# Kernel optimization log

Measured on AMD Instinct MI355X. Metric: run time of the kernel, lower is better.

## Reference

```python
import jax, jax.numpy as jnp
import numpy as np

B, T, RES, C = 4, 8, 32, 128
TSP, SPLIT = 4, 4
NH_BRANCH = 4  # num_heads // 2 per branch
HID = 4 * C


def layer_norm(x, w, b, eps=1e-5):
    mu = x.mean(-1, keepdims=True)
    var = ((x - mu) ** 2).mean(-1, keepdims=True)
    return (x - mu) * jax.lax.rsqrt(var + eps) * w + b


def dwconv3d(x, w, b):
    # x: (Bw, C, Tsp, Hsp, Wsp); w: (C, 1, 3, 3, 3) depthwise
    y = jax.lax.conv_general_dilated(
        x, w, (1, 1, 1), 'SAME',
        dimension_numbers=('NCDHW', 'OIDHW', 'NCDHW'),
        feature_group_count=x.shape[1])
    return y + b[None, :, None, None, None]


def lepe_attention(q, k, v, conv_w, conv_b, Tsp, Hsp, Wsp, nh, Tt, H, W):
    Bq, L, Cc = q.shape
    hd = Cc // nh
    win = Tsp * Hsp * Wsp
    scale = float(hd) ** -0.5

    def to_win(z):
        z = z.reshape(Bq, Tt // Tsp, Tsp, H // Hsp, Hsp, W // Wsp, Wsp, Cc)
        z = z.transpose(0, 1, 3, 5, 2, 4, 6, 7).reshape(-1, win, nh, hd)
        return z.transpose(0, 2, 1, 3)

    qw = to_win(q) * scale
    kw = to_win(k)
    # v windows as (Bw, C, Tsp, Hsp, Wsp) for the depthwise-conv LePE
    vw5 = v.reshape(Bq, Tt // Tsp, Tsp, H // Hsp, Hsp, W // Wsp, Wsp, Cc)
    vw5 = vw5.transpose(0, 1, 3, 5, 7, 2, 4, 6).reshape(-1, Cc, Tsp, Hsp, Wsp)
    lepe = dwconv3d(vw5, conv_w, conv_b)

    def heads(z5):
        return z5.reshape(-1, nh, hd, win).transpose(0, 1, 3, 2)

    vh, lepeh = heads(vw5), heads(lepe)
    attn = jax.nn.softmax(jnp.einsum('bnqd,bnkd->bnqk', qw, kw), axis=-1)
    out = jnp.einsum('bnqk,bnkd->bnqd', attn, vh) + lepeh
    # windows -> video token order (T, H, W)
    out = out.transpose(0, 2, 1, 3).reshape(
        Bq, Tt // Tsp, H // Hsp, W // Wsp, Tsp, Hsp, Wsp, Cc)
    out = out.transpose(0, 1, 4, 2, 5, 3, 6, 7).reshape(Bq, L, Cc)
    return out


def setup_inputs() -> dict:
    key = jax.random.key(0)
    ks = jax.random.split(key, 16)
    L = T * RES * RES
    h = C // 2
    p = lambda k, s: jax.random.normal(k, s, dtype=jnp.float32) * 0.02
    return {
        'x': jax.random.normal(ks[0], (B, L, C), dtype=jnp.float32),
        'norm1_w': jnp.ones((C,), jnp.float32),
        'norm1_b': jnp.zeros((C,), jnp.float32),
        'qkv_w': p(ks[1], (3 * C, C)),
        'conv_w0': p(ks[2], (h, 1, 3, 3, 3)),
        'conv_b0': jnp.zeros((h,), jnp.float32),
        'conv_w1': p(ks[3], (h, 1, 3, 3, 3)),
        'conv_b1': jnp.zeros((h,), jnp.float32),
        'proj_w': p(ks[4], (C, C)),
        'proj_b': jnp.zeros((C,), jnp.float32),
        'norm2_w': jnp.ones((C,), jnp.float32),
        'norm2_b': jnp.zeros((C,), jnp.float32),
        'fc1_w': p(ks[5], (HID, C)),
        'fc1_b': jnp.zeros((HID,), jnp.float32),
        'fc2_w': p(ks[6], (C, HID)),
        'fc2_b': jnp.zeros((C,), jnp.float32),
    }


def reference(x, norm1_w, norm1_b, qkv_w, conv_w0, conv_b0, conv_w1, conv_b1,
              proj_w, proj_b, norm2_w, norm2_b, fc1_w, fc1_b, fc2_w, fc2_b):
    img = layer_norm(x, norm1_w, norm1_b)
    qkv = img @ qkv_w.T  # (B, L, 3C), split order q, k, v
    q, k, v = jnp.split(qkv, 3, axis=-1)
    h = C // 2
    # branch 0 (idx=0): H_sp = reso, W_sp = split_size
    x1 = lepe_attention(q[..., :h], k[..., :h], v[..., :h], conv_w0, conv_b0,
                        TSP, RES, SPLIT, NH_BRANCH, T, RES, RES)
    # branch 1 (idx=1): H_sp = split_size, W_sp = reso
    x2 = lepe_attention(q[..., h:], k[..., h:], v[..., h:], conv_w1, conv_b1,
                        TSP, SPLIT, RES, NH_BRANCH, T, RES, RES)
    att = jnp.concatenate([x1, x2], axis=2) @ proj_w.T + proj_b
    x = x + att
    y = layer_norm(x, norm2_w, norm2_b)
    y = jax.nn.gelu(y @ fc1_w.T + fc1_b, approximate=False) @ fc2_w.T + fc2_b
    return x + y
```

## Files before the change

kernel.cpp:

```cpp
#include <hip/hip_runtime.h>
#include <math.h>

namespace {
constexpr int C_ = 128;
constexpr int BL = 32768;
constexpr int LS = 140;

typedef __attribute__((ext_vector_type(4))) float f32x4;
typedef __attribute__((ext_vector_type(4))) _Float16 f16x4;
typedef __attribute__((ext_vector_type(8))) _Float16 f16x8;
typedef __attribute__((ext_vector_type(2))) __fp16 hf2;

#if __has_builtin(__builtin_amdgcn_exp2f)
#define EXP2F(x) __builtin_amdgcn_exp2f(x)
#else
#define EXP2F(x) exp2f(x)
#endif
}

__global__ __launch_bounds__(256) void k_cvt(
    const float* __restrict__ qkvw, const float* __restrict__ pw,
    const float* __restrict__ f1w,  const float* __restrict__ f2w,
    const float* __restrict__ cw0,  const float* __restrict__ cw1,
    _Float16* __restrict__ wqh, _Float16* __restrict__ pwh,
    _Float16* __restrict__ w1h, _Float16* __restrict__ w2h,
    float* __restrict__ lepw)
{
  int i = blockIdx.x * 256 + threadIdx.x;
  if (i < 49152) {
    float v = qkvw[i];
    if (i < 16384) v *= 0.360673762f;
    wqh[i] = (_Float16)v;
  }
  else if (i < 65536)  pwh[i - 49152] = (_Float16)pw[i - 49152];
  else if (i < 131072) w1h[i - 65536] = (_Float16)f1w[i - 65536];
  else if (i < 196608) w2h[i - 131072] = (_Float16)f2w[i - 131072];
  else if (i < 200064) {
    int j = i - 196608;
    int br = j / 1728, r = j % 1728, widx = r >> 6, ch = r & 63;
    lepw[j] = (br ? cw1 : cw0)[ch * 27 + widx];
  }
}

__global__ __launch_bounds__(512) void k_ln_qkv(
    const float* __restrict__ x,
    const float* __restrict__ nw,
    const float* __restrict__ nb,
    const _Float16* __restrict__ wqh,
    _Float16* __restrict__ qh, _Float16* __restrict__ kh, _Float16* __restrict__ vh)
{
  __shared__ _Float16 xs[64][LS];
  __shared__ _Float16 qt[64][LS];
  __shared__ _Float16 wbuf[128][LS];
  const int tid = threadIdx.x;
  const int row0 = blockIdx.x << 6;
  const int bb = row0 >> 13, t = (row0 >> 10) & 7, h0 = (row0 >> 5) & 31;
  const int tb = t >> 2, t_in = t & 3;

  {
    const int r = tid >> 3, j = tid & 7;
    const float* xp = x + (size_t)(row0 + r) * C_ + j * 16;
    float v[16];
#pragma unroll
    for (int i = 0; i < 4; ++i) {
      float4 u = ((const float4*)xp)[i];
      v[i*4+0] = u.x; v[i*4+1] = u.y; v[i*4+2] = u.z; v[i*4+3] = u.w;
    }
    float s1 = 0.f, s2 = 0.f;
#pragma unroll
    for (int i = 0; i < 16; ++i) { s1 += v[i]; s2 += v[i] * v[i]; }
    s1 += __shfl_down(s1, 4, 8); s1 += __shfl_down(s1, 2, 8); s1 += __shfl_down(s1, 1, 8);
    s2 += __shfl_down(s2, 4, 8); s2 += __shfl_down(s2, 2, 8); s2 += __shfl_down(s2, 1, 8);
    float mu = __shfl(s1, 0, 8) * (1.f / 128.f);
    float ms = __shfl(s2, 0, 8) * (1.f / 128.f);
    float rstd = rsqrtf(ms - mu * mu + 1e-5f);
#pragma unroll
    for (int i = 0; i < 16; ++i) {
      int c = j * 16 + i;
      xs[r][c] = (_Float16)((v[i] - mu) * rstd * nw[c] + nb[c]);
    }
  }
  __syncthreads();

  const int lane = tid & 63, wave = tid >> 6;
  const int mq = wave & 3, nh = wave >> 2;
  const int m0 = mq << 4, mi = lane & 15, quad = lane >> 4;

  f16x8 afr[4];
#pragma unroll
  for (int kt = 0; kt < 4; ++kt)
    afr[kt] = *(const f16x8*)&xs[m0 + mi][kt * 32 + quad * 8];

  for (int g = 0; g < 3; ++g) {
#pragma unroll
    for (int it = 0; it < 4; ++it) {
      int id = it * 512 + tid;
      int r = id >> 4, c8 = id & 15;
      *(uint4*)&wbuf[r][c8 * 8] = *(const uint4*)(wqh + (size_t)(g * 128 + r) * 128 + c8 * 8);
    }
    __syncthreads();

    f32x4 acc[4];
#pragma unroll
    for (int nt = 0; nt < 4; ++nt) acc[nt] = (f32x4){0.f, 0.f, 0.f, 0.f};
#pragma unroll
    for (int nt = 0; nt < 4; ++nt) {
      int wrow = (nh * 4 + nt) * 16 + mi;
#pragma unroll
      for (int kt = 0; kt < 4; ++kt) {
        f16x8 bfr = *(const f16x8*)&wbuf[wrow][kt * 32 + quad * 8];
        acc[nt] = __builtin_amdgcn_mfma_f32_16x16x32_f16(afr[kt], bfr, acc[nt], 0, 0, 0);
      }
    }
#pragma unroll
    for (int nt = 0; nt < 4; ++nt) {
      int n = (nh * 4 + nt) * 16 + mi;
#pragma unroll
      for (int rr = 0; rr < 4; ++rr)
        qt[m0 + quad * 4 + rr][n] = (_Float16)acc[nt][rr];
    }
    __syncthreads();

    _Float16* G = (g == 0) ? qh : (g == 1) ? kh : vh;
#pragma unroll
    for (int it = 0; it < 2; ++it) {
      int u = it * 512 + tid;
      if (u < 512) {
        int half = u & 1, p = (u >> 1) & 7, head = (u >> 4) & 3, sb = u >> 6;
        int token = (p >> 2) * 32 + sb * 4 + (p & 3);
        uint4 d = *(const uint4*)&qt[token][head * 16 + half * 8];
        int win = bb * 16 + tb * 8 + sb;
        int pos = t_in * 128 + h0 * 4 + p;
        *(uint4*)(G + ((size_t)(head * 64 + win) * 512 + pos) * 16 + half * 8) = d;
      } else {
        int u2 = u - 512;
        int half = u2 & 1, pin = (u2 >> 1) & 63, head = u2 >> 7;
        uint4 d = *(const uint4*)&qt[pin][64 + head * 16 + half * 8];
        int win = bb * 16 + tb * 8 + (h0 >> 2);
        int pos = t_in * 128 + (h0 & 3) * 32 + pin;
        *(uint4*)(G + ((size_t)((4 + head) * 64 + win) * 512 + pos) * 16 + half * 8) = d;
      }
    }
    __syncthreads();
  }
}

__global__ __launch_bounds__(512) void k_attn(
    const _Float16* __restrict__ qh,
    const _Float16* __restrict__ kh,
    const _Float16* __restrict__ vh,
    const float* __restrict__ lepw,
    const float* __restrict__ cb0,
    const float* __restrict__ cb1,
    _Float16* __restrict__ attnh)
{
  __shared__ _Float16 Ks[512][20];
  __shared__ _Float16 Vs[512][20];
  __shared__ _Float16 Vt[16][520];

  const int tid = threadIdx.x;
  const int bid = blockIdx.x;
  const int br = bid >> 8, wi = (bid >> 2) & 63, head = bid & 3;
  const int b = wi >> 4, tb = (wi >> 3) & 1, sb = wi & 7;
  const int coff = br * 64 + head * 16;
  const int Hsp = br ? 4 : 32, Wsp = br ? 32 : 4;
  const float* cb = br ? cb1 : cb0;
  const size_t base = ((size_t)(br * 4 + head) * 64 + wi) * 512 * 16;

  auto token_of = [&](int p) -> int {
    int t_in = p >> 7;
    int rem = p & 127;
    int h, w;
    if (br == 0) { h = rem >> 2;            w = sb * 4 + (rem & 3); }
    else         { h = sb * 4 + (rem >> 5); w = rem & 31; }
    return ((b * 8 + tb * 4 + t_in) << 10) + (h << 5) + w;
  };

  {
    const int r = tid;
    const _Float16* kp = kh + base + r * 16;
    const _Float16* vp = vh + base + r * 16;
    f16x8 k0 = *(const f16x8*)kp;
    f16x8 k1 = *(const f16x8*)(kp + 8);
    f16x8 v0 = *(const f16x8*)vp;
    f16x8 v1 = *(const f16x8*)(vp + 8);
    *(f16x4*)&Ks[r][0]  = (f16x4){k0[0], k0[1], k0[2], k0[3]};
    *(f16x4*)&Ks[r][4]  = (f16x4){k0[4], k0[5], k0[6], k0[7]};
    *(f16x4*)&Ks[r][8]  = (f16x4){k1[0], k1[1], k1[2], k1[3]};
    *(f16x4*)&Ks[r][12] = (f16x4){k1[4], k1[5], k1[6], k1[7]};
    *(f16x4*)&Vs[r][0]  = (f16x4){v0[0], v0[1], v0[2], v0[3]};
    *(f16x4*)&Vs[r][4]  = (f16x4){v0[4], v0[5], v0[6], v0[7]};
    *(f16x4*)&Vs[r][8]  = (f16x4){v1[0], v1[1], v1[2], v1[3]};
    *(f16x4*)&Vs[r][12] = (f16x4){v1[4], v1[5], v1[6], v1[7]};
#pragma unroll
    for (int d = 0; d < 8; ++d) { Vt[d][r] = v0[d]; Vt[d + 8][r] = v1[d]; }
  }

  const int lane = tid & 63, wave = tid >> 6;
  const int mi = lane & 15, quad = lane >> 4;

  int qtok[4];
  f16x4 qfr[4];
#pragma unroll
  for (int qi = 0; qi < 4; ++qi) {
    int q = (wave * 4 + qi) * 16 + mi;
    qtok[qi] = token_of(q);
    qfr[qi] = *(const f16x4*)(qh + base + q * 16 + quad * 4);
  }
  __syncthreads();

  f32x4 acc[4];
  float l[4];
#pragma unroll
  for (int qi = 0; qi < 4; ++qi) { acc[qi] = (f32x4){0.f,0.f,0.f,0.f}; l[qi] = 0.f; }

  const hf2 one2 = {(__fp16)1.f, (__fp16)1.f};

  for (int kt = 0; kt < 32; ++kt) {
    const int kb = kt << 4;
    f16x4 kfr = *(const f16x4*)&Ks[kb + mi][quad * 4];
    f16x4 vfr = *(const f16x4*)&Vt[mi][kb + quad * 4];
#pragma unroll
    for (int qi = 0; qi < 4; ++qi) {
      f32x4 s = __builtin_amdgcn_mfma_f32_16x16x16f16(kfr, qfr[qi], (f32x4){0.f,0.f,0.f,0.f}, 0, 0, 0);
      float p0 = EXP2F(s[0]);
      float p1 = EXP2F(s[1]);
      float p2 = EXP2F(s[2]);
      float p3 = EXP2F(s[3]);
      hf2 plo = __builtin_amdgcn_cvt_pkrtz(p0, p1);
      hf2 phi = __builtin_amdgcn_cvt_pkrtz(p2, p3);
#if __has_builtin(__builtin_amdgcn_fdot2)
      l[qi] = __builtin_amdgcn_fdot2(plo, one2, l[qi], false);
      l[qi] = __builtin_amdgcn_fdot2(phi, one2, l[qi], false);
#else
      l[qi] += (p0 + p1) + (p2 + p3);
#endif
      union { struct { hf2 lo, hi; } h; f16x4 v; } u;
      u.h.lo = plo; u.h.hi = phi;
      acc[qi] = __builtin_amdgcn_mfma_f32_16x16x16f16(vfr, u.v, acc[qi], 0, 0, 0);
    }
  }

#pragma unroll
  for (int qi = 0; qi < 4; ++qi) {
    float lq = l[qi];
    lq += __shfl_xor(lq, 16, 64);
    lq += __shfl_xor(lq, 32, 64);
    float inv = 1.f / lq;

    const int q = (wave * 4 + qi) * 16 + mi;
    int t_in = q >> 7, rem = q & 127;
    int h_in, w_in;
    if (br == 0) { h_in = rem >> 2; w_in = rem & 3; }
    else         { h_in = rem >> 5; w_in = rem & 31; }
    float4 lep = *(const float4*)(cb + head * 16 + quad * 4);
    for (int dz = 0; dz < 3; ++dz) {
      int tz = t_in + dz - 1; if ((unsigned)tz >= 4u) continue;
      for (int dy = 0; dy < 3; ++dy) {
        int ty = h_in + dy - 1; if ((unsigned)ty >= (unsigned)Hsp) continue;
        for (int dx = 0; dx < 3; ++dx) {
          int tx = w_in + dx - 1; if ((unsigned)tx >= (unsigned)Wsp) continue;
          int np = (tz * Hsp + ty) * Wsp + tx;
          int widx = (dz * 3 + dy) * 3 + dx;
          float4 w4 = *(const float4*)(lepw + ((br * 27 + widx) << 6) + head * 16 + quad * 4);
          f16x4 vv = *(const f16x4*)&Vs[np][quad * 4];
          lep.x += w4.x * (float)vv[0];
          lep.y += w4.y * (float)vv[1];
          lep.z += w4.z * (float)vv[2];
          lep.w += w4.w * (float)vv[3];
        }
      }
    }
    f16x4 ov;
    ov[0] = (_Float16)(acc[qi][0] * inv + lep.x);
    ov[1] = (_Float16)(acc[qi][1] * inv + lep.y);
    ov[2] = (_Float16)(acc[qi][2] * inv + lep.z);
    ov[3] = (_Float16)(acc[qi][3] * inv + lep.w);
    *(f16x4*)(attnh + (size_t)qtok[qi] * 128 + coff + quad * 4) = ov;
  }
}

__global__ __launch_bounds__(512) void k_proj(
    const _Float16* __restrict__ attnh,
    const _Float16* __restrict__ pwh,
    const float* __restrict__ pb,
    const float* __restrict__ x,
    _Float16* __restrict__ xrh)
{
  __shared__ _Float16 as_[64][LS];
  __shared__ _Float16 wbuf[128][LS];
  const int tid = threadIdx.x;
  const int row0 = blockIdx.x << 6;

#pragma unroll
  for (int it = 0; it < 2; ++it) {
    int id = it * 512 + tid;
    int r = id >> 4, c8 = id & 15;
    *(uint4*)&as_[r][c8 * 8] = *(const uint4*)(attnh + (size_t)(row0 + r) * 128 + c8 * 8);
  }
#pragma unroll
  for (int it = 0; it < 4; ++it) {
    int id = it * 512 + tid;
    int r = id >> 4, c8 = id & 15;
    *(uint4*)&wbuf[r][c8 * 8] = *(const uint4*)(pwh + (size_t)r * 128 + c8 * 8);
  }
  __syncthreads();

  const int lane = tid & 63, wave = tid >> 6;
  const int mq = wave & 3, nh = wave >> 2;
  const int m0 = mq << 4, mi = lane & 15, quad = lane >> 4;

  f16x8 afr[4];
#pragma unroll
  for (int kt = 0; kt < 4; ++kt)
    afr[kt] = *(const f16x8*)&as_[m0 + mi][kt * 32 + quad * 8];

  f32x4 acc[4];
#pragma unroll
  for (int nt = 0; nt < 4; ++nt) acc[nt] = (f32x4){0.f, 0.f, 0.f, 0.f};
#pragma unroll
  for (int nt = 0; nt < 4; ++nt) {
    int wrow = (nh * 4 + nt) * 16 + mi;
#pragma unroll
    for (int kt = 0; kt < 4; ++kt) {
      f16x8 bfr = *(const f16x8*)&wbuf[wrow][kt * 32 + quad * 8];
      acc[nt] = __builtin_amdgcn_mfma_f32_16x16x32_f16(afr[kt], bfr, acc[nt], 0, 0, 0);
    }
  }
  __syncthreads();
#pragma unroll
  for (int nt = 0; nt < 4; ++nt) {
    int n = (nh * 4 + nt) * 16 + mi;
    float bb = pb[n];
#pragma unroll
    for (int rr = 0; rr < 4; ++rr)
      as_[m0 + quad * 4 + rr][n] = (_Float16)(acc[nt][rr] + bb);
  }
  __syncthreads();

#pragma unroll
  for (int it = 0; it < 2; ++it) {
    int id = it * 512 + tid;
    int r = id >> 4, c8 = id & 15;
    f16x8 v = *(const f16x8*)&as_[r][c8 * 8];
    const float* xp = x + (size_t)(row0 + r) * 128 + c8 * 8;
    float4 xa = *(const float4*)xp;
    float4 xb = *(const float4*)(xp + 4);
    f16x8 o;
    o[0] = (_Float16)((float)v[0] + xa.x); o[1] = (_Float16)((float)v[1] + xa.y);
    o[2] = (_Float16)((float)v[2] + xa.z); o[3] = (_Float16)((float)v[3] + xa.w);
    o[4] = (_Float16)((float)v[4] + xb.x); o[5] = (_Float16)((float)v[5] + xb.y);
    o[6] = (_Float16)((float)v[6] + xb.z); o[7] = (_Float16)((float)v[7] + xb.w);
    *(f16x8*)(xrh + (size_t)(row0 + r) * 128 + c8 * 8) = o;
  }
}

__global__ __launch_bounds__(512) void k_mlp(
    const _Float16* __restrict__ xrh,
    const float* __restrict__ nw,
    const float* __restrict__ nb,
    const _Float16* __restrict__ w1h,
    const float* __restrict__ f1b,
    const _Float16* __restrict__ w2h,
    const float* __restrict__ f2b,
    float* __restrict__ out)
{
  __shared__ _Float16 xs[64][LS];
  __shared__ _Float16 wbuf[128][LS];
  const int tid = threadIdx.x;
  const int row0 = blockIdx.x << 6;

  {
    const int r = tid >> 3, j = tid & 7;
    const _Float16* xp = xrh + (size_t)(row0 + r) * C_ + j * 16;
    float v[16];
#pragma unroll
    for (int i = 0; i < 2; ++i) {
      f16x8 u = ((const f16x8*)xp)[i];
#pragma unroll
      for (int k = 0; k < 8; ++k) v[i * 8 + k] = (float)u[k];
    }
    float s1 = 0.f, s2 = 0.f;
#pragma unroll
    for (int i = 0; i < 16; ++i) { s1 += v[i]; s2 += v[i] * v[i]; }
    s1 += __shfl_down(s1, 4, 8); s1 += __shfl_down(s1, 2, 8); s1 += __shfl_down(s1, 1, 8);
    s2 += __shfl_down(s2, 4, 8); s2 += __shfl_down(s2, 2, 8); s2 += __shfl_down(s2, 1, 8);
    float mu = __shfl(s1, 0, 8) * (1.f / 128.f);
    float ms = __shfl(s2, 0, 8) * (1.f / 128.f);
    float rstd = rsqrtf(ms - mu * mu + 1e-5f);
#pragma unroll
    for (int i = 0; i < 16; ++i) {
      int c = j * 16 + i;
      xs[r][c] = (_Float16)((v[i] - mu) * rstd * nw[c] + nb[c]);
    }
  }
  __syncthreads();

  const int lane = tid & 63, wave = tid >> 6;
  const int mt = wave & 3, hh = wave >> 2;
  const int tok0 = mt << 4, mi = lane & 15, quad = lane >> 4;

  f16x8 bx[4];
#pragma unroll
  for (int kt = 0; kt < 4; ++kt)
    bx[kt] = *(const f16x8*)&xs[tok0 + mi][kt * 32 + quad * 8];

  f32x4 oacc[8];
#pragma unroll
  for (int o = 0; o < 8; ++o) oacc[o] = (f32x4){0.f, 0.f, 0.f, 0.f};

  auto gelu = [](float h) -> float {
    return h * __frcp_rn(1.f + EXP2F(-2.4554774f * h));
  };

  for (int ng = 0; ng < 4; ++ng) {
#pragma unroll
    for (int it = 0; it < 4; ++it) {
      int id = it * 512 + tid;
      int r = id >> 4, c8 = id & 15;
      *(uint4*)&wbuf[r][c8 * 8] = *(const uint4*)(w1h + (size_t)(ng * 128 + r) * 128 + c8 * 8);
    }
    __syncthreads();

    f32x4 hacc[4];
#pragma unroll
    for (int t = 0; t < 4; ++t) hacc[t] = (f32x4){0.f, 0.f, 0.f, 0.f};
#pragma unroll
    for (int t = 0; t < 4; ++t) {
      int hrow = hh * 64 + t * 16 + mi;
#pragma unroll
      for (int kt = 0; kt < 4; ++kt) {
        f16x8 wfr = *(const f16x8*)&wbuf[hrow][kt * 32 + quad * 8];
        hacc[t] = __builtin_amdgcn_mfma_f32_16x16x32_f16(wfr, bx[kt], hacc[t], 0, 0, 0);
      }
    }
    f16x4 ph[4];
#pragma unroll
    for (int t = 0; t < 4; ++t) {
      float4 bj = *(const float4*)(f1b + ng * 128 + hh * 64 + t * 16 + quad * 4);
      ph[t][0] = (_Float16)gelu(hacc[t][0] + bj.x);
      ph[t][1] = (_Float16)gelu(hacc[t][1] + bj.y);
      ph[t][2] = (_Float16)gelu(hacc[t][2] + bj.z);
      ph[t][3] = (_Float16)gelu(hacc[t][3] + bj.w);
    }
    __syncthreads();

#pragma unroll
    for (int it = 0; it < 4; ++it) {
      int id = it * 512 + tid;
      int r = id >> 4, c8 = id & 15;
      *(uint4*)&wbuf[r][c8 * 8] = *(const uint4*)(w2h + (size_t)r * 512 + ng * 128 + c8 * 8);
    }
    __syncthreads();

#pragma unroll
    for (int o = 0; o < 8; ++o) {
#pragma unroll
      for (int t = 0; t < 4; ++t) {
        f16x4 wfr = *(const f16x4*)&wbuf[o * 16 + mi][(hh * 4 + t) * 16 + quad * 4];
        oacc[o] = __builtin_amdgcn_mfma_f32_16x16x16f16(wfr, ph[t], oacc[o], 0, 0, 0);
      }
    }
    __syncthreads();
  }

  float* rbuf = (float*)wbuf;
  if (hh == 1) {
#pragma unroll
    for (int o = 0; o < 8; ++o)
#pragma unroll
      for (int k = 0; k < 4; ++k)
        rbuf[(o * 4 + k) * 256 + mt * 64 + lane] = oacc[o][k];
  }
  __syncthreads();
  if (hh == 0) {
#pragma unroll
    for (int o = 0; o < 8; ++o)
#pragma unroll
      for (int k = 0; k < 4; ++k)
        oacc[o][k] += rbuf[(o * 4 + k) * 256 + mt * 64 + lane];

#pragma unroll
    for (int o = 0; o < 8; ++o) {
      int row = row0 + tok0 + mi;
      int cb4 = o * 16 + quad * 4;
      float4 bo = *(const float4*)(f2b + cb4);
      f16x4 res = *(const f16x4*)(xrh + (size_t)row * C_ + cb4);
      float4 ov;
      ov.x = oacc[o][0] + bo.x + (float)res[0];
      ov.y = oacc[o][1] + bo.y + (float)res[1];
      ov.z = oacc[o][2] + bo.z + (float)res[2];
      ov.w = oacc[o][3] + bo.w + (float)res[3];
      *(float4*)(out + (size_t)row * C_ + cb4) = ov;
    }
  }
}

extern "C" void kernel_launch(void* const* d_in, const int* in_sizes, int n_in,
                              void* d_out, int out_size, void* d_ws, size_t ws_size,
                              hipStream_t stream)
{
  const float* x    = (const float*)d_in[0];
  const float* n1w  = (const float*)d_in[1];
  const float* n1b  = (const float*)d_in[2];
  const float* qkvw = (const float*)d_in[3];
  const float* cw0  = (const float*)d_in[4];
  const float* cb0  = (const float*)d_in[5];
  const float* cw1  = (const float*)d_in[6];
  const float* cb1  = (const float*)d_in[7];
  const float* pw   = (const float*)d_in[8];
  const float* pb   = (const float*)d_in[9];
  const float* n2w  = (const float*)d_in[10];
  const float* n2b  = (const float*)d_in[11];
  const float* f1w  = (const float*)d_in[12];
  const float* f1b  = (const float*)d_in[13];
  const float* f2w  = (const float*)d_in[14];
  const float* f2b  = (const float*)d_in[15];

  char* ws = (char*)d_ws;
  _Float16* qh    = (_Float16*)ws;
  _Float16* kh    = (_Float16*)(ws +  8388608);
  _Float16* vh    = (_Float16*)(ws + 16777216);
  _Float16* attnh = (_Float16*)(ws + 25165824);
  _Float16* xrh   = (_Float16*)(ws + 33554432);
  _Float16* wqh   = (_Float16*)(ws + 41943040);
  _Float16* pwh   = (_Float16*)(ws + 42041344);
  _Float16* w1h   = (_Float16*)(ws + 42074112);
  _Float16* w2h   = (_Float16*)(ws + 42205184);
  float*    lepw  = (float*)   (ws + 42336256);

  k_cvt   <<<782,      256, 0, stream>>>(qkvw, pw, f1w, f2w, cw0, cw1,
                                         wqh, pwh, w1h, w2h, lepw);
  k_ln_qkv<<<BL / 64,  512, 0, stream>>>(x, n1w, n1b, wqh, qh, kh, vh);
  k_attn  <<<512,      512, 0, stream>>>(qh, kh, vh, lepw, cb0, cb1, attnh);
  k_proj  <<<BL / 64,  512, 0, stream>>>(attnh, pwh, pb, x, xrh);
  k_mlp   <<<BL / 64,  512, 0, stream>>>(xrh, n2w, n2b, w1h, f1b, w2h, f2b,
                                         (float*)d_out);
}
```

Measured before the change: 181.2 us.

## Fuse output projection and MLP into one kernel keeping residual in LDS

Merges the projection kernel and the MLP kernel into a single kernel per 64-row tile. The post-attention residual stays in shared memory instead of making a round trip through a global fp16 buffer, and one kernel launch goes away. In exchange the kernel uses an extra 64x140 fp16 LDS buffer, which may lower occupancy, and the proj output write gains an extra barrier.

Result: faster. 175.5 us, median of 2 (-3.1%).

```diff
diff --git a/kernel.cpp b/kernel.cpp
--- a/kernel.cpp
+++ b/kernel.cpp
@@ -280,17 +280,26 @@
   }
 }
 
-__global__ __launch_bounds__(512) void k_proj(
+__global__ __launch_bounds__(512) void k_pm(
     const _Float16* __restrict__ attnh,
     const _Float16* __restrict__ pwh,
     const float* __restrict__ pb,
     const float* __restrict__ x,
-    _Float16* __restrict__ xrh)
+    const float* __restrict__ nw,
+    const float* __restrict__ nb,
+    const _Float16* __restrict__ w1h,
+    const float* __restrict__ f1b,
+    const _Float16* __restrict__ w2h,
+    const float* __restrict__ f2b,
+    float* __restrict__ out)
 {
   __shared__ _Float16 as_[64][LS];
   __shared__ _Float16 wbuf[128][LS];
+  __shared__ _Float16 xrb[64][LS];
   const int tid = threadIdx.x;
   const int row0 = blockIdx.x << 6;
+  const int lane = tid & 63, wave = tid >> 6;
+  const int mi = lane & 15, quad = lane >> 4;
 
 #pragma unroll
   for (int it = 0; it < 2; ++it) {
@@ -306,35 +315,35 @@
   }
   __syncthreads();
 
-  const int lane = tid & 63, wave = tid >> 6;
-  const int mq = wave & 3, nh = wave >> 2;
-  const int m0 = mq << 4, mi = lane & 15, quad = lane >> 4;
-
-  f16x8 afr[4];
-#pragma unroll
-  for (int kt = 0; kt < 4; ++kt)
-    afr[kt] = *(const f16x8*)&as_[m0 + mi][kt * 32 + quad * 8];
-
-  f32x4 acc[4];
-#pragma unroll
-  for (int nt = 0; nt < 4; ++nt) acc[nt] = (f32x4){0.f, 0.f, 0.f, 0.f};
-#pragma unroll
-  for (int nt = 0; nt < 4; ++nt) {
-    int wrow = (nh * 4 + nt) * 16 + mi;
-#pragma unroll
-    for (int kt = 0; kt < 4; ++kt) {
-      f16x8 bfr = *(const f16x8*)&wbuf[wrow][kt * 32 + quad * 8];
-      acc[nt] = __builtin_amdgcn_mfma_f32_16x16x32_f16(afr[kt], bfr, acc[nt], 0, 0, 0);
-    }
-  }
-  __syncthreads();
-#pragma unroll
-  for (int nt = 0; nt < 4; ++nt) {
-    int n = (nh * 4 + nt) * 16 + mi;
-    float bb = pb[n];
-#pragma unroll
-    for (int rr = 0; rr < 4; ++rr)
-      as_[m0 + quad * 4 + rr][n] = (_Float16)(acc[nt][rr] + bb);
+  {
+    const int mq = wave & 3, nh = wave >> 2;
+    const int m0 = mq << 4;
+
+    f16x8 afr[4];
+#pragma unroll
+    for (int kt = 0; kt < 4; ++kt)
+      afr[kt] = *(const f16x8*)&as_[m0 + mi][kt * 32 + quad * 8];
+
+    f32x4 acc[4];
+#pragma unroll
+    for (int nt = 0; nt < 4; ++nt) acc[nt] = (f32x4){0.f, 0.f, 0.f, 0.f};
+#pragma unroll
+    for (int nt = 0; nt < 4; ++nt) {
+      int wrow = (nh * 4 + nt) * 16 + mi;
+#pragma unroll
+      for (int kt = 0; kt < 4; ++kt) {
+        f16x8 bfr = *(const f16x8*)&wbuf[wrow][kt * 32 + quad * 8];
+        acc[nt] = __builtin_amdgcn_mfma_f32_16x16x32_f16(afr[kt], bfr, acc[nt], 0, 0, 0);
+      }
+    }
+#pragma unroll
+    for (int nt = 0; nt < 4; ++nt) {
+      int n = (nh * 4 + nt) * 16 + mi;
+      float bb = pb[n];
+#pragma unroll
+      for (int rr = 0; rr < 4; ++rr)
+        xrb[m0 + quad * 4 + rr][n] = (_Float16)(acc[nt][rr] + bb);
+    }
   }
   __syncthreads();
 
@@ -342,7 +351,7 @@
   for (int it = 0; it < 2; ++it) {
     int id = it * 512 + tid;
     int r = id >> 4, c8 = id & 15;
-    f16x8 v = *(const f16x8*)&as_[r][c8 * 8];
+    f16x8 v = *(const f16x8*)&xrb[r][c8 * 8];
     const float* xp = x + (size_t)(row0 + r) * 128 + c8 * 8;
     float4 xa = *(const float4*)xp;
     float4 xb = *(const float4*)(xp + 4);
@@ -351,32 +360,16 @@
     o[2] = (_Float16)((float)v[2] + xa.z); o[3] = (_Float16)((float)v[3] + xa.w);
     o[4] = (_Float16)((float)v[4] + xb.x); o[5] = (_Float16)((float)v[5] + xb.y);
     o[6] = (_Float16)((float)v[6] + xb.z); o[7] = (_Float16)((float)v[7] + xb.w);
-    *(f16x8*)(xrh + (size_t)(row0 + r) * 128 + c8 * 8) = o;
-  }
-}
-
-__global__ __launch_bounds__(512) void k_mlp(
-    const _Float16* __restrict__ xrh,
-    const float* __restrict__ nw,
-    const float* __restrict__ nb,
-    const _Float16* __restrict__ w1h,
-    const float* __restrict__ f1b,
-    const _Float16* __restrict__ w2h,
-    const float* __restrict__ f2b,
-    float* __restrict__ out)
-{
-  __shared__ _Float16 xs[64][LS];
-  __shared__ _Float16 wbuf[128][LS];
-  const int tid = threadIdx.x;
-  const int row0 = blockIdx.x << 6;
+    *(f16x8*)&xrb[r][c8 * 8] = o;
+  }
+  __syncthreads();
 
   {
     const int r = tid >> 3, j = tid & 7;
-    const _Float16* xp = xrh + (size_t)(row0 + r) * C_ + j * 16;
     float v[16];
 #pragma unroll
     for (int i = 0; i < 2; ++i) {
-      f16x8 u = ((const f16x8*)xp)[i];
+      f16x8 u = *(const f16x8*)&xrb[r][j * 16 + i * 8];
 #pragma unroll
       for (int k = 0; k < 8; ++k) v[i * 8 + k] = (float)u[k];
     }
@@ -391,19 +384,18 @@
 #pragma unroll
     for (int i = 0; i < 16; ++i) {
       int c = j * 16 + i;
-      xs[r][c] = (_Float16)((v[i] - mu) * rstd * nw[c] + nb[c]);
-    }
-  }
-  __syncthreads();
-
-  const int lane = tid & 63, wave = tid >> 6;
+      as_[r][c] = (_Float16)((v[i] - mu) * rstd * nw[c] + nb[c]);
+    }
+  }
+  __syncthreads();
+
   const int mt = wave & 3, hh = wave >> 2;
-  const int tok0 = mt << 4, mi = lane & 15, quad = lane >> 4;
+  const int tok0 = mt << 4;
 
   f16x8 bx[4];
 #pragma unroll
   for (int kt = 0; kt < 4; ++kt)
-    bx[kt] = *(const f16x8*)&xs[tok0 + mi][kt * 32 + quad * 8];
+    bx[kt] = *(const f16x8*)&as_[tok0 + mi][kt * 32 + quad * 8];
 
   f32x4 oacc[8];
 #pragma unroll
@@ -485,7 +477,7 @@
       int row = row0 + tok0 + mi;
       int cb4 = o * 16 + quad * 4;
       float4 bo = *(const float4*)(f2b + cb4);
-      f16x4 res = *(const f16x4*)(xrh + (size_t)row * C_ + cb4);
+      f16x4 res = *(const f16x4*)&xrb[tok0 + mi][cb4];
       float4 ov;
       ov.x = oacc[o][0] + bo.x + (float)res[0];
       ov.y = oacc[o][1] + bo.y + (float)res[1];
@@ -522,18 +514,16 @@
   _Float16* kh    = (_Float16*)(ws +  8388608);
   _Float16* vh    = (_Float16*)(ws + 16777216);
   _Float16* attnh = (_Float16*)(ws + 25165824);
-  _Float16* xrh   = (_Float16*)(ws + 33554432);
-  _Float16* wqh   = (_Float16*)(ws + 41943040);
-  _Float16* pwh   = (_Float16*)(ws + 42041344);
-  _Float16* w1h   = (_Float16*)(ws + 42074112);
-  _Float16* w2h   = (_Float16*)(ws + 42205184);
-  float*    lepw  = (float*)   (ws + 42336256);
+  _Float16* wqh   = (_Float16*)(ws + 33554432);
+  _Float16* pwh   = (_Float16*)(ws + 33652736);
+  _Float16* w1h   = (_Float16*)(ws + 33685504);
+  _Float16* w2h   = (_Float16*)(ws + 33816576);
+  float*    lepw  = (float*)   (ws + 33947648);
 
   k_cvt   <<<782,      256, 0, stream>>>(qkvw, pw, f1w, f2w, cw0, cw1,
                                          wqh, pwh, w1h, w2h, lepw);
   k_ln_qkv<<<BL / 64,  512, 0, stream>>>(x, n1w, n1b, wqh, qh, kh, vh);
   k_attn  <<<512,      512, 0, stream>>>(qh, kh, vh, lepw, cb0, cb1, attnh);
-  k_proj  <<<BL / 64,  512, 0, stream>>>(attnh, pwh, pb, x, xrh);
-  k_mlp   <<<BL / 64,  512, 0, stream>>>(xrh, n2w, n2b, w1h, f1b, w2h, f2b,
-                                         (float*)d_out);
+  k_pm    <<<BL / 64,  512, 0, stream>>>(attnh, pwh, pb, x, n2w, n2b,
+                                         w1h, f1b, w2h, f2b, (float*)d_out);
 }
```
